# Optimization experiments

Hardware: AMD Instinct MI355X
Metric: run time of the kernel (lower is better)

## Reference

```python
import jax, jax.numpy as jnp
import numpy as np

B, C, D, H, W = 8, 256, 128, 64, 64  # batch, in_channels, inter_dim, spatial
BN_EPS = 1e-5


def setup_inputs() -> dict:
    key = jax.random.key(0)
    ks = jax.random.split(key, 6)
    s_c = 1.0 / np.sqrt(C)
    s_d = 1.0 / np.sqrt(D)
    return {
        "x": jax.random.normal(ks[0], (B, C, H, W), dtype=jnp.float32),
        # 1x1 conv kernels, stored as [out_ch, in_ch]
        "theta_w": jax.random.normal(ks[1], (D, C), dtype=jnp.float32) * s_c,
        "phi_w": jax.random.normal(ks[2], (D, C), dtype=jnp.float32) * s_c,
        "g_w": jax.random.normal(ks[3], (D, C), dtype=jnp.float32) * s_c,
        "w_w": jax.random.normal(ks[4], (C, D), dtype=jnp.float32) * s_d,
        "w_b": jnp.zeros((C,), dtype=jnp.float32),
        "bn_gamma": jnp.ones((C,), dtype=jnp.float32),
        "bn_beta": jnp.zeros((C,), dtype=jnp.float32),
    }


def reference(x, theta_w, phi_w, g_w, w_w, w_b, bn_gamma, bn_beta):
    Bs, Cs, Hs, Ws = x.shape
    N = Hs * Ws
    xf = x.reshape(Bs, Cs, N)  # flatten spatial -> [B, C, N]

    # 1x1 convs (bias=False) == per-position channel matmuls
    theta = jnp.einsum('dc,bcn->bnd', theta_w, xf)  # [B, N, D]
    phi = jnp.einsum('dc,bcn->bdn', phi_w, xf)      # [B, D, N]
    g = jnp.einsum('dc,bcn->bnd', g_w, xf)          # [B, N, D]

    # embedded-Gaussian attention: softmax(theta @ phi) @ g
    f = jnp.einsum('bnd,bdm->bnm', theta, phi)      # [B, N, N]
    f_div_C = jax.nn.softmax(f, axis=-1)
    y = jnp.einsum('bnm,bmd->bnd', f_div_C, g)      # [B, N, D]

    # output projection W (1x1 conv with bias)
    w_y = jnp.einsum('cd,bnd->bcn', w_w, y) + w_b[None, :, None]  # [B, C, N]

    # BatchNorm (training mode: batch statistics, biased variance)
    mean = w_y.mean(axis=(0, 2))
    var = jnp.mean(jnp.square(w_y - mean[None, :, None]), axis=(0, 2))
    scale = (bn_gamma * jax.lax.rsqrt(var + BN_EPS))[None, :, None]
    w_y = (w_y - mean[None, :, None]) * scale + bn_beta[None, :, None]

    z = w_y + xf  # residual
    return z.reshape(Bs, Cs, Hs, Ws)
```

## Files before the change

kernel.cpp:

```cpp
#include <hip/hip_runtime.h>

#define BB 8
#define CC 256
#define DD 128
#define NN 4096
#define BN_EPS 1e-5f

typedef _Float16 f16;
typedef _Float16 half8 __attribute__((ext_vector_type(8)));
typedef _Float16 half2t __attribute__((ext_vector_type(2)));
typedef float f32x4 __attribute__((ext_vector_type(4)));

__device__ __forceinline__ f32x4 mfma16(half8 a, half8 b, f32x4 c) {
  return __builtin_amdgcn_mfma_f32_16x16x32_f16(a, b, c, 0, 0, 0);
}

__device__ __forceinline__ void gload_lds16(const void* g, void* l) {
  __builtin_amdgcn_global_load_lds((const __attribute__((address_space(1))) void*)g,
                                   (__attribute__((address_space(3))) void*)l, 16, 0, 0);
}

__device__ __forceinline__ half2t pkrtz(float a, float b) {
  auto t = __builtin_amdgcn_cvt_pkrtz(a, b);
  return __builtin_bit_cast(half2t, t);
}

#define EXP2(x) __builtin_amdgcn_exp2f(x)

#define PERM(i) ((((i) >> 5) & 1) * 32 + (((i) >> 2) & 3) * 8 + (((i) >> 4) & 1) * 4 + ((i) & 3))

__global__ void k_cast_weights(const float* __restrict__ tw, const float* __restrict__ pw,
                               const float* __restrict__ gw, const float* __restrict__ ww,
                               f16* __restrict__ Wcat, f16* __restrict__ Wwh,
                               float* __restrict__ stats) {
  int i = blockIdx.x * 256 + threadIdx.x;
  if (i < 32768) Wcat[i] = (f16)tw[i];
  else if (i < 65536) Wcat[i] = (f16)pw[i - 32768];
  else if (i < 98304) Wcat[i] = (f16)gw[i - 65536];
  else if (i < 131072) Wwh[i - 98304] = (f16)ww[i - 98304];
  if (i < 512) stats[i] = 0.f;
}

__global__ void k_transpose_x(const float* __restrict__ x, f16* __restrict__ xT) {
  __shared__ f16 tile[32][33];
  int b = blockIdx.z, c0 = blockIdx.y * 32, n0 = blockIdx.x * 32;
  int tx = threadIdx.x, ty = threadIdx.y;
  const float* xp = x + ((size_t)b * CC + c0) * NN + n0;
  for (int j = 0; j < 4; ++j) {
    int cc = ty + j * 8;
    tile[cc][tx] = (f16)xp[(size_t)cc * NN + tx];
  }
  __syncthreads();
  f16* xo = xT + ((size_t)b * NN + n0) * CC + c0;
  for (int j = 0; j < 4; ++j) {
    int nn = ty + j * 8;
    xo[(size_t)nn * CC + tx] = tile[tx][nn];
  }
}

__global__ __launch_bounds__(256) void k_gemm1(const f16* __restrict__ xT, const f16* __restrict__ Wcat,
                                               f16* __restrict__ T, f16* __restrict__ P,
                                               f16* __restrict__ Gnd) {
  int b = blockIdx.y;
  int lane = threadIdx.x & 63, wave = threadIdx.x >> 6;
  int lr = lane & 15, lg = lane >> 4;
  int wr = wave >> 1, wc = wave & 1;
  int m0 = blockIdx.x * 64 + wr * 32;
  const f16* A = xT + (size_t)b * NN * CC;
  half8 a[2][8];
#pragma unroll
  for (int i = 0; i < 2; ++i)
#pragma unroll
    for (int k0 = 0; k0 < 8; ++k0)
      a[i][k0] = *(const half8*)(A + (size_t)(m0 + i * 16 + lr) * CC + k0 * 32 + lg * 8);
  size_t base = (size_t)b * NN;
#pragma unroll
  for (int yb = 0; yb < 6; ++yb) {
    int c0 = yb * 64 + wc * 32;
    f32x4 acc[2][2] = {};
#pragma unroll
    for (int k0 = 0; k0 < 8; ++k0) {
      half8 w[2];
      for (int j = 0; j < 2; ++j)
        w[j] = *(const half8*)(Wcat + (size_t)(c0 + j * 16 + lr) * CC + k0 * 32 + lg * 8);
      for (int i = 0; i < 2; ++i)
        for (int j = 0; j < 2; ++j)
          acc[i][j] = mfma16(a[i][k0], w[j], acc[i][j]);
    }
    f16* dst = (yb < 2) ? T : (yb < 4) ? P : Gnd;
    int cl0 = (yb & 1) * 64 + wc * 32;
    for (int i = 0; i < 2; ++i)
      for (int j = 0; j < 2; ++j)
        for (int r = 0; r < 4; ++r) {
          int row = m0 + i * 16 + lg * 4 + r;
          int col = cl0 + j * 16 + lr;
          dst[(base + row) * DD + col] = (f16)acc[i][j][r];
        }
  }
}

__global__ void k_transpose_g(const f16* __restrict__ Gnd, f16* __restrict__ Gdn) {
  __shared__ f16 tile[32][33];
  int b = blockIdx.z, d0 = blockIdx.y * 32, n0 = blockIdx.x * 32;
  int tx = threadIdx.x, ty = threadIdx.y;
  for (int j = 0; j < 4; ++j) {
    int nn = ty + j * 8;
    tile[nn][tx] = Gnd[((size_t)b * NN + n0 + nn) * DD + d0 + tx];
  }
  __syncthreads();
  for (int j = 0; j < 4; ++j) {
    int dd = ty + j * 8;
    Gdn[((size_t)b * DD + d0 + dd) * NN + n0 + tx] = tile[tx][dd];
  }
}

__global__ __launch_bounds__(256) void k_flash(const f16* __restrict__ T, const f16* __restrict__ P,
                                               const f16* __restrict__ Gdn, f16* __restrict__ Y) {
  __shared__ char smem[65536];
  int bid = blockIdx.x;
  int b = bid & 7;
  int qx = bid >> 3;
  int tid = threadIdx.x;
  int lane = tid & 63, wave = tid >> 6;
  int lr = lane & 15, lg = lane >> 4;
  int q0 = qx * 64 + wave * 16;
  const f16* Tb = T + (size_t)b * NN * DD;
  const f16* Pb = P + (size_t)b * NN * DD;
  const f16* Vb = Gdn + (size_t)b * DD * NN;
  int srcq = 4 * lg;

  const f16* kbase[4];
  const f16* vbase[4];
  char* kdst[4];
  char* vdst[4];
#pragma unroll
  for (int inst = 0; inst < 4; ++inst) {
    int t = inst * 256 + tid;
    int row = t >> 4, sp = t & 15, sl = sp ^ (row & 7);
    kbase[inst] = Pb + (size_t)PERM(row) * DD + sl * 8;
    kdst[inst] = smem + (inst * 256 + wave * 64) * 16;
    int rv = t >> 3, spv = t & 7, slv = spv ^ (rv & 7);
    vbase[inst] = Vb + (size_t)rv * NN + slv * 8;
    vdst[inst] = smem + 32768 + (inst * 256 + wave * 64) * 16;
  }

  half8 qf[4];
  for (int ks = 0; ks < 4; ++ks) {
    half8 v = *(const half8*)(Tb + (size_t)(q0 + lr) * DD + ks * 32 + lg * 8);
    for (int j = 0; j < 8; ++j) v[j] *= (f16)1.44269504f;
    qf[ks] = v;
  }
  half8 ones;
  for (int j = 0; j < 8; ++j) ones[j] = (f16)1.f;

  f32x4 acc[8] = {};
  f32x4 lsum = {};
  float m_run = -1e30f;

#pragma unroll
  for (int inst = 0; inst < 4; ++inst) gload_lds16(kbase[inst], kdst[inst]);
#pragma unroll
  for (int inst = 0; inst < 4; ++inst) gload_lds16(vbase[inst], vdst[inst]);

  for (int kb = 0; kb < 64; ++kb) {
    int keyn = (kb < 63) ? kb * 64 + 64 : 0;
    int cur = (kb & 1) * 16384, nxt = ((kb + 1) & 1) * 16384;
    char* Kc = smem + cur;
    char* Vc = smem + 32768 + cur;

    size_t ko = (size_t)keyn * DD;
#pragma unroll
    for (int inst = 0; inst < 4; ++inst) gload_lds16(kbase[inst] + ko, kdst[inst] + nxt);
    asm volatile("s_waitcnt vmcnt(8)" ::: "memory");
    __builtin_amdgcn_sched_barrier(0);
    __builtin_amdgcn_s_barrier();
    __builtin_amdgcn_sched_barrier(0);

    f32x4 s[4];
    __builtin_amdgcn_s_setprio(1);
    for (int kt = 0; kt < 4; ++kt) {
      f32x4 t = {};
      for (int ks = 0; ks < 4; ++ks) {
        half8 kf = *(const half8*)(Kc + (kt * 16 + lr) * 256 + (((ks * 4 + lg) ^ (lr & 7)) << 4));
        t = mfma16(kf, qf[ks], t);
      }
      s[kt] = t;
    }
    __builtin_amdgcn_s_setprio(0);

    float mA = fmaxf(fmaxf(s[0][0], s[0][1]), s[0][2]);
    mA = fmaxf(fmaxf(mA, s[0][3]), s[1][0]);
    mA = fmaxf(fmaxf(mA, s[1][1]), s[1][2]);
    mA = fmaxf(mA, s[1][3]);
    float mB = fmaxf(fmaxf(s[2][0], s[2][1]), s[2][2]);
    mB = fmaxf(fmaxf(mB, s[2][3]), s[3][0]);
    mB = fmaxf(fmaxf(mB, s[3][1]), s[3][2]);
    mB = fmaxf(mB, s[3][3]);
    float mx = fmaxf(mA, mB);
    mx = fmaxf(mx, __shfl_xor(mx, 16));
    mx = fmaxf(mx, __shfl_xor(mx, 32));
    bool grow = mx > m_run + 11.5f;
    if (__ballot(grow)) {
      float mn = fmaxf(m_run, mx);
      float corr = EXP2(m_run - mn);
      m_run = mn;
      float c0 = __shfl(corr, srcq + 0), c1 = __shfl(corr, srcq + 1);
      float c2 = __shfl(corr, srcq + 2), c3 = __shfl(corr, srcq + 3);
      lsum[0] *= c0; lsum[1] *= c1; lsum[2] *= c2; lsum[3] *= c3;
      for (int nb = 0; nb < 8; ++nb) {
        acc[nb][0] *= c0; acc[nb][1] *= c1; acc[nb][2] *= c2; acc[nb][3] *= c3;
      }
    }
    for (int kt = 0; kt < 4; ++kt)
      for (int r = 0; r < 4; ++r)
        s[kt][r] = EXP2(s[kt][r] - m_run);

    half8 af[2];
    for (int kst = 0; kst < 2; ++kst) {
      union { half8 h8; half2t h2[4]; } un;
      un.h2[0] = pkrtz(s[2 * kst][0], s[2 * kst][1]);
      un.h2[1] = pkrtz(s[2 * kst][2], s[2 * kst][3]);
      un.h2[2] = pkrtz(s[2 * kst + 1][0], s[2 * kst + 1][1]);
      un.h2[3] = pkrtz(s[2 * kst + 1][2], s[2 * kst + 1][3]);
      af[kst] = un.h8;
    }
    lsum = mfma16(af[0], ones, lsum);
    lsum = mfma16(af[1], ones, lsum);

#pragma unroll
    for (int inst = 0; inst < 4; ++inst) gload_lds16(vbase[inst] + keyn, vdst[inst] + nxt);
    asm volatile("s_waitcnt vmcnt(8)" ::: "memory");
    __builtin_amdgcn_sched_barrier(0);
    __builtin_amdgcn_s_barrier();
    __builtin_amdgcn_sched_barrier(0);

    __builtin_amdgcn_s_setprio(1);
    for (int nb = 0; nb < 8; ++nb)
      for (int kst = 0; kst < 2; ++kst) {
        half8 vf = *(const half8*)(Vc + (nb * 16 + lr) * 128 + (((kst * 4 + lg) ^ (lr & 7)) << 4));
        acc[nb] = mfma16(af[kst], vf, acc[nb]);
      }
    __builtin_amdgcn_s_setprio(0);
  }
  asm volatile("s_waitcnt vmcnt(0)" ::: "memory");

  float il[4];
  for (int r = 0; r < 4; ++r) il[r] = 1.f / lsum[r];
  f16* Yb = Y + (size_t)b * NN * DD;
  for (int nb = 0; nb < 8; ++nb)
    for (int r = 0; r < 4; ++r)
      Yb[(size_t)(q0 + lg * 4 + r) * DD + nb * 16 + lr] = (f16)(acc[nb][r] * il[r]);
}

__global__ __launch_bounds__(256) void k_gemm2(const f16* __restrict__ Y, const f16* __restrict__ Wwh,
                                               const float* __restrict__ wb, f16* __restrict__ wy,
                                               float* __restrict__ stats) {
  __shared__ float part[2][8][64];
  int lane = threadIdx.x & 63, wave = threadIdx.x >> 6;
  int lr = lane & 15, lg = lane >> 4;
  int wr = wave >> 1, wc = wave & 1;
  int c0 = blockIdx.y * 64 + wc * 32;
  half8 w[4][2];
  for (int k0 = 0; k0 < 4; ++k0)
    for (int j = 0; j < 2; ++j)
      w[k0][j] = *(const half8*)(Wwh + (size_t)(c0 + j * 16 + lr) * DD + k0 * 32 + lg * 8);
  float bias[2];
  for (int j = 0; j < 2; ++j) bias[j] = wb[c0 + j * 16 + lr];
  float ps[2][2] = {};
  for (int mt = 0; mt < 8; ++mt) {
    int m0 = (blockIdx.x * 8 + mt) * 64 + wr * 32;
    f32x4 acc[2][2] = {};
    for (int k0 = 0; k0 < 4; ++k0) {
      half8 a[2];
      for (int i = 0; i < 2; ++i)
        a[i] = *(const half8*)(Y + (size_t)(m0 + i * 16 + lr) * DD + k0 * 32 + lg * 8);
      for (int i = 0; i < 2; ++i)
        for (int j = 0; j < 2; ++j)
          acc[i][j] = mfma16(a[i], w[k0][j], acc[i][j]);
    }
    for (int i = 0; i < 2; ++i)
      for (int j = 0; j < 2; ++j)
        for (int r = 0; r < 4; ++r) {
          int row = m0 + i * 16 + lg * 4 + r;
          int col = c0 + j * 16 + lr;
          float v = acc[i][j][r] + bias[j];
          wy[(size_t)row * CC + col] = (f16)v;
          ps[j][0] += v;
          ps[j][1] += v * v;
        }
  }
  for (int j = 0; j < 2; ++j) {
    int colL = wc * 32 + j * 16 + lr;
    part[0][wr * 4 + lg][colL] = ps[j][0];
    part[1][wr * 4 + lg][colL] = ps[j][1];
  }
  __syncthreads();
  if (threadIdx.x < 128) {
    int metric = threadIdx.x >> 6, col = threadIdx.x & 63;
    float s = 0.f;
    for (int wtr = 0; wtr < 8; ++wtr) s += part[metric][wtr][col];
    atomicAdd(&stats[metric * CC + blockIdx.y * 64 + col], s);
  }
}

__global__ void k_bn_apply(const f16* __restrict__ wy, const float* __restrict__ x,
                           const float* __restrict__ stats, const float* __restrict__ gamma,
                           const float* __restrict__ beta, float* __restrict__ out) {
  __shared__ f16 tile[32][33];
  int b = blockIdx.z, c0 = blockIdx.y * 32, n0 = blockIdx.x * 32;
  int tx = threadIdx.x, ty = threadIdx.y;
  for (int j = 0; j < 4; ++j) {
    int nn = ty + j * 8;
    tile[nn][tx] = wy[((size_t)b * NN + n0 + nn) * CC + c0 + tx];
  }
  __syncthreads();
  const float inv_cnt = 1.f / (float)(BB * NN);
  for (int j = 0; j < 4; ++j) {
    int cc = ty + j * 8;
    int c = c0 + cc;
    float mean = stats[c] * inv_cnt;
    float var = stats[CC + c] * inv_cnt - mean * mean;
    float scale = gamma[c] * rsqrtf(var + BN_EPS);
    size_t oi = ((size_t)b * CC + c) * NN + n0 + tx;
    out[oi] = ((float)tile[tx][cc] - mean) * scale + beta[c] + x[oi];
  }
}

extern "C" void kernel_launch(void* const* d_in, const int* in_sizes, int n_in,
                              void* d_out, int out_size, void* d_ws, size_t ws_size,
                              hipStream_t stream) {
  const float* x = (const float*)d_in[0];
  const float* tw = (const float*)d_in[1];
  const float* pw = (const float*)d_in[2];
  const float* gw = (const float*)d_in[3];
  const float* ww = (const float*)d_in[4];
  const float* wb = (const float*)d_in[5];
  const float* gamma = (const float*)d_in[6];
  const float* beta = (const float*)d_in[7];
  float* out = (float*)d_out;
  char* ws = (char*)d_ws;

  f16* Wcat = (f16*)(ws + 0);
  f16* Wwh = (f16*)(ws + 196608);
  float* stats = (float*)(ws + 262144);
  const size_t BASE = 1 << 20;
  f16* T = (f16*)(ws + BASE);
  f16* P = (f16*)(ws + BASE + 8388608);
  f16* Gdn = (f16*)(ws + BASE + 16777216);
  f16* Yb = (f16*)(ws + BASE + 25165824);
  f16* xT = (f16*)(ws + BASE + 33554432);
  f16* Gnd = (f16*)(ws + BASE + 50331648);
  f16* wy = (f16*)(ws + BASE + 33554432);

  k_cast_weights<<<512, 256, 0, stream>>>(tw, pw, gw, ww, Wcat, Wwh, stats);
  k_transpose_x<<<dim3(NN / 32, CC / 32, BB), dim3(32, 8), 0, stream>>>(x, xT);
  k_gemm1<<<dim3(NN / 64, BB), 256, 0, stream>>>(xT, Wcat, T, P, Gnd);
  k_transpose_g<<<dim3(NN / 32, DD / 32, BB), dim3(32, 8), 0, stream>>>(Gnd, Gdn);
  k_flash<<<512, 256, 0, stream>>>(T, P, Gdn, Yb);
  k_gemm2<<<dim3(BB * NN / 512, CC / 64), 256, 0, stream>>>(Yb, Wwh, wb, wy, stats);
  k_bn_apply<<<dim3(NN / 32, CC / 32, BB), dim3(32, 8), 0, stream>>>(wy, x, stats, gamma, beta, out);
}
```

Baseline: 182.3 us.

## Split flash attention over key halves with merge kernel; fuse transposes into gemm1

The attention kernel is split along the key dimension into two halves: 1024 blocks each handle 32-key tiles over 2048 keys, using half the LDS and a launch_bounds occupancy hint. Each half writes an unnormalized partial output along with its running max and sum, and a new merge kernel combines the two halves with a log-sum-exp rescale. Separately, the x transpose and G transpose kernels are removed: gemm1 now reads fp32 x directly, converts and transposes it through swizzled LDS, and writes G already transposed. This cuts two launches and an intermediate round trip, and improves occupancy and parallelism in the attention kernel. In exchange it adds a partial-result write, a merge pass, and smaller MFMA tiles per barrier.

```diff
diff --git a/kernel.cpp b/kernel.cpp
--- a/kernel.cpp
+++ b/kernel.cpp
@@ -27,7 +27,7 @@
 
 #define EXP2(x) __builtin_amdgcn_exp2f(x)
 
-#define PERM(i) ((((i) >> 5) & 1) * 32 + (((i) >> 2) & 3) * 8 + (((i) >> 4) & 1) * 4 + ((i) & 3))
+#define PERM32(i) ((((i) >> 2) & 3) * 8 + (((i) >> 4) & 1) * 4 + ((i) & 3))
 
 __global__ void k_cast_weights(const float* __restrict__ tw, const float* __restrict__ pw,
                                const float* __restrict__ gw, const float* __restrict__ ww,
@@ -41,39 +41,43 @@
   if (i < 512) stats[i] = 0.f;
 }
 
-__global__ void k_transpose_x(const float* __restrict__ x, f16* __restrict__ xT) {
-  __shared__ f16 tile[32][33];
-  int b = blockIdx.z, c0 = blockIdx.y * 32, n0 = blockIdx.x * 32;
-  int tx = threadIdx.x, ty = threadIdx.y;
-  const float* xp = x + ((size_t)b * CC + c0) * NN + n0;
-  for (int j = 0; j < 4; ++j) {
-    int cc = ty + j * 8;
-    tile[cc][tx] = (f16)xp[(size_t)cc * NN + tx];
-  }
-  __syncthreads();
-  f16* xo = xT + ((size_t)b * NN + n0) * CC + c0;
-  for (int j = 0; j < 4; ++j) {
-    int nn = ty + j * 8;
-    xo[(size_t)nn * CC + tx] = tile[tx][nn];
-  }
-}
-
-__global__ __launch_bounds__(256) void k_gemm1(const f16* __restrict__ xT, const f16* __restrict__ Wcat,
+__global__ __launch_bounds__(256) void k_gemm1(const float* __restrict__ x, const f16* __restrict__ Wcat,
                                                f16* __restrict__ T, f16* __restrict__ P,
-                                               f16* __restrict__ Gnd) {
+                                               f16* __restrict__ Gdn) {
+  __shared__ char xls[32768];
+  __shared__ char gls[16384];
   int b = blockIdx.y;
-  int lane = threadIdx.x & 63, wave = threadIdx.x >> 6;
+  int n0 = blockIdx.x * 64;
+  int tid = threadIdx.x;
+  int lane = tid & 63, wave = tid >> 6;
   int lr = lane & 15, lg = lane >> 4;
   int wr = wave >> 1, wc = wave & 1;
-  int m0 = blockIdx.x * 64 + wr * 32;
-  const f16* A = xT + (size_t)b * NN * CC;
+
+  {
+    int c = tid;
+    const float* src = x + ((size_t)b * CC + c) * NN + n0;
+#pragma unroll
+    for (int n4 = 0; n4 < 64; n4 += 4) {
+      f32x4 v = *(const f32x4*)(src + n4);
+#pragma unroll
+      for (int k = 0; k < 4; ++k) {
+        int n = n4 + k;
+        *(f16*)(xls + n * 512 + ((((c >> 3) ^ (n & 7)) * 8 + (c & 7)) * 2)) = (f16)v[k];
+      }
+    }
+  }
+  __syncthreads();
+
   half8 a[2][8];
 #pragma unroll
-  for (int i = 0; i < 2; ++i)
+  for (int i = 0; i < 2; ++i) {
+    int nloc = wr * 32 + i * 16 + lr;
 #pragma unroll
     for (int k0 = 0; k0 < 8; ++k0)
-      a[i][k0] = *(const half8*)(A + (size_t)(m0 + i * 16 + lr) * CC + k0 * 32 + lg * 8);
-  size_t base = (size_t)b * NN;
+      a[i][k0] = *(const half8*)(xls + nloc * 512 + (((k0 * 4 + lg) ^ (nloc & 7)) << 4));
+  }
+
+  size_t base = (size_t)b * NN + n0;
 #pragma unroll
   for (int yb = 0; yb < 6; ++yb) {
     int c0 = yb * 64 + wc * 32;
@@ -87,61 +91,73 @@
         for (int j = 0; j < 2; ++j)
           acc[i][j] = mfma16(a[i][k0], w[j], acc[i][j]);
     }
-    f16* dst = (yb < 2) ? T : (yb < 4) ? P : Gnd;
-    int cl0 = (yb & 1) * 64 + wc * 32;
-    for (int i = 0; i < 2; ++i)
-      for (int j = 0; j < 2; ++j)
-        for (int r = 0; r < 4; ++r) {
-          int row = m0 + i * 16 + lg * 4 + r;
-          int col = cl0 + j * 16 + lr;
-          dst[(base + row) * DD + col] = (f16)acc[i][j][r];
-        }
-  }
-}
-
-__global__ void k_transpose_g(const f16* __restrict__ Gnd, f16* __restrict__ Gdn) {
-  __shared__ f16 tile[32][33];
-  int b = blockIdx.z, d0 = blockIdx.y * 32, n0 = blockIdx.x * 32;
-  int tx = threadIdx.x, ty = threadIdx.y;
-  for (int j = 0; j < 4; ++j) {
-    int nn = ty + j * 8;
-    tile[nn][tx] = Gnd[((size_t)b * NN + n0 + nn) * DD + d0 + tx];
+    if (yb < 4) {
+      f16* dst = (yb < 2) ? T : P;
+      int cl0 = (yb & 1) * 64 + wc * 32;
+      for (int i = 0; i < 2; ++i)
+        for (int j = 0; j < 2; ++j)
+          for (int r = 0; r < 4; ++r) {
+            int row = wr * 32 + i * 16 + lg * 4 + r;
+            int col = cl0 + j * 16 + lr;
+            dst[(base + row) * DD + col] = (f16)acc[i][j][r];
+          }
+    } else {
+      for (int i = 0; i < 2; ++i)
+        for (int j = 0; j < 2; ++j)
+          for (int r = 0; r < 4; ++r) {
+            int n = wr * 32 + i * 16 + lg * 4 + r;
+            int d = (yb - 4) * 64 + wc * 32 + j * 16 + lr;
+            *(f16*)(gls + n * 256 + ((((d >> 3) ^ (n & 7)) * 8 + (d & 7)) * 2)) = (f16)acc[i][j][r];
+          }
+    }
   }
   __syncthreads();
-  for (int j = 0; j < 4; ++j) {
-    int dd = ty + j * 8;
-    Gdn[((size_t)b * DD + d0 + dd) * NN + n0 + tx] = tile[tx][dd];
-  }
-}
-
-__global__ __launch_bounds__(256) void k_flash(const f16* __restrict__ T, const f16* __restrict__ P,
-                                               const f16* __restrict__ Gdn, f16* __restrict__ Y) {
-  __shared__ char smem[65536];
+  {
+    int d = tid >> 1, nh = (tid & 1) * 32;
+    f16 tmp[32];
+#pragma unroll
+    for (int k = 0; k < 32; ++k) {
+      int n = nh + k;
+      tmp[k] = *(const f16*)(gls + n * 256 + ((((d >> 3) ^ (n & 7)) * 8 + (d & 7)) * 2));
+    }
+    f16* dst = Gdn + ((size_t)b * DD + d) * NN + n0 + nh;
+#pragma unroll
+    for (int k = 0; k < 4; ++k)
+      *(half8*)(dst + k * 8) = *(const half8*)(tmp + k * 8);
+  }
+}
+
+__global__ __launch_bounds__(256, 4) void k_flash(const f16* __restrict__ T, const f16* __restrict__ P,
+                                                  const f16* __restrict__ Gdn, f16* __restrict__ acc0,
+                                                  f16* __restrict__ acc1, float* __restrict__ ml) {
+  __shared__ char smem[32768];
   int bid = blockIdx.x;
   int b = bid & 7;
-  int qx = bid >> 3;
+  int u = bid >> 3;
+  int hf = u & 1;
+  int qx = u >> 1;
   int tid = threadIdx.x;
   int lane = tid & 63, wave = tid >> 6;
   int lr = lane & 15, lg = lane >> 4;
   int q0 = qx * 64 + wave * 16;
   const f16* Tb = T + (size_t)b * NN * DD;
-  const f16* Pb = P + (size_t)b * NN * DD;
-  const f16* Vb = Gdn + (size_t)b * DD * NN;
+  const f16* Pb = P + ((size_t)b * NN + hf * 2048) * DD;
+  const f16* Vb = Gdn + (size_t)b * DD * NN + hf * 2048;
   int srcq = 4 * lg;
 
-  const f16* kbase[4];
-  const f16* vbase[4];
-  char* kdst[4];
-  char* vdst[4];
-#pragma unroll
-  for (int inst = 0; inst < 4; ++inst) {
+  const f16* kbase[2];
+  const f16* vbase[2];
+  char* kdst[2];
+  char* vdst[2];
+#pragma unroll
+  for (int inst = 0; inst < 2; ++inst) {
     int t = inst * 256 + tid;
     int row = t >> 4, sp = t & 15, sl = sp ^ (row & 7);
-    kbase[inst] = Pb + (size_t)PERM(row) * DD + sl * 8;
+    kbase[inst] = Pb + (size_t)PERM32(row) * DD + sl * 8;
     kdst[inst] = smem + (inst * 256 + wave * 64) * 16;
-    int rv = t >> 3, spv = t & 7, slv = spv ^ (rv & 7);
-    vbase[inst] = Vb + (size_t)rv * NN + slv * 8;
-    vdst[inst] = smem + 32768 + (inst * 256 + wave * 64) * 16;
+    int dv = t >> 2, gv = t & 3, glv = gv ^ ((dv >> 1) & 3);
+    vbase[inst] = Vb + (size_t)dv * NN + glv * 8;
+    vdst[inst] = smem + 16384 + (inst * 256 + wave * 64) * 16;
   }
 
   half8 qf[4];
@@ -158,27 +174,27 @@
   float m_run = -1e30f;
 
 #pragma unroll
-  for (int inst = 0; inst < 4; ++inst) gload_lds16(kbase[inst], kdst[inst]);
-#pragma unroll
-  for (int inst = 0; inst < 4; ++inst) gload_lds16(vbase[inst], vdst[inst]);
+  for (int inst = 0; inst < 2; ++inst) gload_lds16(kbase[inst], kdst[inst]);
+#pragma unroll
+  for (int inst = 0; inst < 2; ++inst) gload_lds16(vbase[inst], vdst[inst]);
 
   for (int kb = 0; kb < 64; ++kb) {
-    int keyn = (kb < 63) ? kb * 64 + 64 : 0;
-    int cur = (kb & 1) * 16384, nxt = ((kb + 1) & 1) * 16384;
+    int keyn = (kb < 63) ? kb * 32 + 32 : 0;
+    int cur = (kb & 1) * 8192, nxt = ((kb + 1) & 1) * 8192;
     char* Kc = smem + cur;
-    char* Vc = smem + 32768 + cur;
+    char* Vc = smem + 16384 + cur;
 
     size_t ko = (size_t)keyn * DD;
 #pragma unroll
-    for (int inst = 0; inst < 4; ++inst) gload_lds16(kbase[inst] + ko, kdst[inst] + nxt);
-    asm volatile("s_waitcnt vmcnt(8)" ::: "memory");
+    for (int inst = 0; inst < 2; ++inst) gload_lds16(kbase[inst] + ko, kdst[inst] + nxt);
+    asm volatile("s_waitcnt vmcnt(4)" ::: "memory");
     __builtin_amdgcn_sched_barrier(0);
     __builtin_amdgcn_s_barrier();
     __builtin_amdgcn_sched_barrier(0);
 
-    f32x4 s[4];
+    f32x4 s[2];
     __builtin_amdgcn_s_setprio(1);
-    for (int kt = 0; kt < 4; ++kt) {
+    for (int kt = 0; kt < 2; ++kt) {
       f32x4 t = {};
       for (int ks = 0; ks < 4; ++ks) {
         half8 kf = *(const half8*)(Kc + (kt * 16 + lr) * 256 + (((ks * 4 + lg) ^ (lr & 7)) << 4));
@@ -188,15 +204,8 @@
     }
     __builtin_amdgcn_s_setprio(0);
 
-    float mA = fmaxf(fmaxf(s[0][0], s[0][1]), s[0][2]);
-    mA = fmaxf(fmaxf(mA, s[0][3]), s[1][0]);
-    mA = fmaxf(fmaxf(mA, s[1][1]), s[1][2]);
-    mA = fmaxf(mA, s[1][3]);
-    float mB = fmaxf(fmaxf(s[2][0], s[2][1]), s[2][2]);
-    mB = fmaxf(fmaxf(mB, s[2][3]), s[3][0]);
-    mB = fmaxf(fmaxf(mB, s[3][1]), s[3][2]);
-    mB = fmaxf(mB, s[3][3]);
-    float mx = fmaxf(mA, mB);
+    float mx = fmaxf(fmaxf(s[0][0], s[0][1]), fmaxf(s[0][2], s[0][3]));
+    mx = fmaxf(mx, fmaxf(fmaxf(s[1][0], s[1][1]), fmaxf(s[1][2], s[1][3])));
     mx = fmaxf(mx, __shfl_xor(mx, 16));
     mx = fmaxf(mx, __shfl_xor(mx, 32));
     bool grow = mx > m_run + 11.5f;
@@ -211,45 +220,65 @@
         acc[nb][0] *= c0; acc[nb][1] *= c1; acc[nb][2] *= c2; acc[nb][3] *= c3;
       }
     }
-    for (int kt = 0; kt < 4; ++kt)
+    for (int kt = 0; kt < 2; ++kt)
       for (int r = 0; r < 4; ++r)
         s[kt][r] = EXP2(s[kt][r] - m_run);
 
-    half8 af[2];
-    for (int kst = 0; kst < 2; ++kst) {
+    half8 af;
+    {
       union { half8 h8; half2t h2[4]; } un;
-      un.h2[0] = pkrtz(s[2 * kst][0], s[2 * kst][1]);
-      un.h2[1] = pkrtz(s[2 * kst][2], s[2 * kst][3]);
-      un.h2[2] = pkrtz(s[2 * kst + 1][0], s[2 * kst + 1][1]);
-      un.h2[3] = pkrtz(s[2 * kst + 1][2], s[2 * kst + 1][3]);
-      af[kst] = un.h8;
-    }
-    lsum = mfma16(af[0], ones, lsum);
-    lsum = mfma16(af[1], ones, lsum);
-
-#pragma unroll
-    for (int inst = 0; inst < 4; ++inst) gload_lds16(vbase[inst] + keyn, vdst[inst] + nxt);
-    asm volatile("s_waitcnt vmcnt(8)" ::: "memory");
+      un.h2[0] = pkrtz(s[0][0], s[0][1]);
+      un.h2[1] = pkrtz(s[0][2], s[0][3]);
+      un.h2[2] = pkrtz(s[1][0], s[1][1]);
+      un.h2[3] = pkrtz(s[1][2], s[1][3]);
+      af = un.h8;
+    }
+    lsum = mfma16(af, ones, lsum);
+
+#pragma unroll
+    for (int inst = 0; inst < 2; ++inst) gload_lds16(vbase[inst] + keyn, vdst[inst] + nxt);
+    asm volatile("s_waitcnt vmcnt(4)" ::: "memory");
     __builtin_amdgcn_sched_barrier(0);
     __builtin_amdgcn_s_barrier();
     __builtin_amdgcn_sched_barrier(0);
 
     __builtin_amdgcn_s_setprio(1);
-    for (int nb = 0; nb < 8; ++nb)
-      for (int kst = 0; kst < 2; ++kst) {
-        half8 vf = *(const half8*)(Vc + (nb * 16 + lr) * 128 + (((kst * 4 + lg) ^ (lr & 7)) << 4));
-        acc[nb] = mfma16(af[kst], vf, acc[nb]);
-      }
+    for (int nb = 0; nb < 8; ++nb) {
+      int d = nb * 16 + lr;
+      half8 vf = *(const half8*)(Vc + d * 64 + ((lg ^ ((d >> 1) & 3)) << 4));
+      acc[nb] = mfma16(af, vf, acc[nb]);
+    }
     __builtin_amdgcn_s_setprio(0);
   }
   asm volatile("s_waitcnt vmcnt(0)" ::: "memory");
 
-  float il[4];
-  for (int r = 0; r < 4; ++r) il[r] = 1.f / lsum[r];
-  f16* Yb = Y + (size_t)b * NN * DD;
+  size_t gq0 = (size_t)b * NN + q0;
+  f16* A = (hf ? acc1 : acc0) + gq0 * DD;
   for (int nb = 0; nb < 8; ++nb)
     for (int r = 0; r < 4; ++r)
-      Yb[(size_t)(q0 + lg * 4 + r) * DD + nb * 16 + lr] = (f16)(acc[nb][r] * il[r]);
+      A[(size_t)(lg * 4 + r) * DD + nb * 16 + lr] = (f16)acc[nb][r];
+  float* mArr = ml + hf * 32768;
+  float* lArr = ml + 65536 + hf * 32768;
+  if (lg == 0) mArr[gq0 + lr] = m_run;
+  if (lr == 0)
+    for (int r = 0; r < 4; ++r) lArr[gq0 + lg * 4 + r] = lsum[r];
+}
+
+__global__ void k_merge(const f16* __restrict__ a0, const f16* __restrict__ a1,
+                        const float* __restrict__ ml, f16* __restrict__ Y) {
+  int idx = blockIdx.x * 256 + threadIdx.x;
+  int q = idx >> 4, dc = (idx & 15) * 8;
+  float m1 = ml[q], m2 = ml[32768 + q];
+  float l1 = ml[65536 + q], l2 = ml[98304 + q];
+  float mm = fmaxf(m1, m2);
+  float c1 = EXP2(m1 - mm), c2 = EXP2(m2 - mm);
+  float inv = 1.f / (l1 * c1 + l2 * c2);
+  c1 *= inv; c2 *= inv;
+  half8 va = *(const half8*)(a0 + (size_t)q * DD + dc);
+  half8 vb = *(const half8*)(a1 + (size_t)q * DD + dc);
+  half8 o;
+  for (int j = 0; j < 8; ++j) o[j] = (f16)((float)va[j] * c1 + (float)vb[j] * c2);
+  *(half8*)(Y + (size_t)q * DD + dc) = o;
 }
 
 __global__ __launch_bounds__(256) void k_gemm2(const f16* __restrict__ Y, const f16* __restrict__ Wwh,
@@ -343,20 +372,19 @@
   f16* Wcat = (f16*)(ws + 0);
   f16* Wwh = (f16*)(ws + 196608);
   float* stats = (float*)(ws + 262144);
+  float* ml = (float*)(ws + 524288);
   const size_t BASE = 1 << 20;
   f16* T = (f16*)(ws + BASE);
   f16* P = (f16*)(ws + BASE + 8388608);
   f16* Gdn = (f16*)(ws + BASE + 16777216);
   f16* Yb = (f16*)(ws + BASE + 25165824);
-  f16* xT = (f16*)(ws + BASE + 33554432);
-  f16* Gnd = (f16*)(ws + BASE + 50331648);
-  f16* wy = (f16*)(ws + BASE + 33554432);
+  f16* acc1 = (f16*)(ws + BASE + 33554432);
+  f16* wy = (f16*)(ws + BASE + 41943040);
 
   k_cast_weights<<<512, 256, 0, stream>>>(tw, pw, gw, ww, Wcat, Wwh, stats);
-  k_transpose_x<<<dim3(NN / 32, CC / 32, BB), dim3(32, 8), 0, stream>>>(x, xT);
-  k_gemm1<<<dim3(NN / 64, BB), 256, 0, stream>>>(xT, Wcat, T, P, Gnd);
-  k_transpose_g<<<dim3(NN / 32, DD / 32, BB), dim3(32, 8), 0, stream>>>(Gnd, Gdn);
-  k_flash<<<512, 256, 0, stream>>>(T, P, Gdn, Yb);
+  k_gemm1<<<dim3(NN / 64, BB), 256, 0, stream>>>(x, Wcat, T, P, Gdn);
+  k_flash<<<1024, 256, 0, stream>>>(T, P, Gdn, Yb, acc1, ml);
+  k_merge<<<2048, 256, 0, stream>>>(Yb, acc1, ml, Yb);
   k_gemm2<<<dim3(BB * NN / 512, CC / 64), 256, 0, stream>>>(Yb, Wwh, wb, wy, stats);
   k_bn_apply<<<dim3(NN / 32, CC / 32, BB), dim3(32, 8), 0, stream>>>(wy, x, stats, gamma, beta, out);
 }
```

Measured after the change: 175.9 us. 3.5% less time.
